# Optimization experiments

Hardware: AMD Instinct MI355X
Metric: run time of the kernel (lower is better)

## Reference

```python
import jax, jax.numpy as jnp
import numpy as np

NHEAD = 8; DM = 512; DFF = 2048; L = 4; S = 1024; NTOK = 51; MLP = 256; CLASSES = 7
GH = 3; GHID = 64; GCLS = 5; ALPHA = 0.2
HD = DM // NHEAD

_ADJ = np.array([[0,1,0,0,0],[1,1,1,1,0],[1,0,1,0,1],[1,0,0,1,1],[0,0,1,1,1]], dtype=np.int32)


def setup_inputs():
    key = jax.random.key(0)
    ks = jax.random.split(key, 24)
    r = lambda k, s, sc=0.05: jax.random.normal(k, s, jnp.float32) * sc
    return {
        'x': jax.random.normal(ks[0], (5, S, NTOK), jnp.float32),
        'adj': jnp.asarray(_ADJ),
        'W_enc': r(ks[1], (NTOK, DM)), 'b_enc': jnp.zeros((DM,), jnp.float32),
        'cls_tok': r(ks[2], (1, 1, DM)),
        'pos_emb': r(ks[3], (S + 1, DM)),
        'Wq': r(ks[4], (L, DM, DM)), 'bq': jnp.zeros((L, DM), jnp.float32),
        'Wk': r(ks[5], (L, DM, DM)), 'bk': jnp.zeros((L, DM), jnp.float32),
        'Wv': r(ks[6], (L, DM, DM)), 'bv': jnp.zeros((L, DM), jnp.float32),
        'Wo': r(ks[7], (L, DM, DM)), 'bo': jnp.zeros((L, DM), jnp.float32),
        'W1': r(ks[8], (L, DM, DFF)), 'b1': jnp.zeros((L, DFF), jnp.float32),
        'W2': r(ks[9], (L, DFF, DM)), 'b2': jnp.zeros((L, DM), jnp.float32),
        'g1': jnp.ones((L, DM), jnp.float32), 'be1': jnp.zeros((L, DM), jnp.float32),
        'g2': jnp.ones((L, DM), jnp.float32), 'be2': jnp.zeros((L, DM), jnp.float32),
        'Wd1': r(ks[10], (DM, MLP)), 'bd1': jnp.zeros((MLP,), jnp.float32),
        'Wd2': r(ks[11], (MLP, CLASSES)), 'bd2': jnp.zeros((CLASSES,), jnp.float32),
        'Wg': r(ks[12], (GH, 3, GHID), 0.3), 'ag': r(ks[13], (GH, 2 * GHID), 0.3),
        'Wgo': r(ks[14], (GH * GHID, GCLS), 0.3), 'ago': r(ks[15], (2 * GCLS,), 0.3),
    }


def _layernorm(x, g, b, eps=1e-5):
    m = x.mean(-1, keepdims=True)
    v = ((x - m) ** 2).mean(-1, keepdims=True)
    return (x - m) * jax.lax.rsqrt(v + eps) * g + b


def _gat_attn_layer(h_in, W, a, mask):
    # standard pyGAT GraphAttentionLayer: e_ij = LeakyReLU(a1.h_i + a2.h_j)
    F = W.shape[1]
    h = h_in @ W                                                    # [N, F]
    e = jax.nn.leaky_relu((h @ a[:F])[:, None] + (h @ a[F:])[None, :], ALPHA)
    att = jax.nn.softmax(jnp.where(mask, e, -9e15), axis=-1)        # adjacency-masked softmax
    return att @ h


def _gat(xg, mask, Wg, ag, Wgo, ago):
    # xg: [5 nodes, 3 feats]; GH attention heads concatenated, then output layer
    heads = jax.vmap(lambda W, a: jax.nn.elu(_gat_attn_layer(xg, W, a, mask)))(Wg, ag)  # [GH,5,GHID]
    hcat = jnp.transpose(heads, (1, 0, 2)).reshape(xg.shape[0], GH * GHID)
    out = jax.nn.elu(_gat_attn_layer(hcat, Wgo, ago, mask))         # [5, GCLS]
    return jax.nn.log_softmax(out, axis=1)


def _forward(x, adj, params):
    (W_enc, b_enc, cls_tok, pos_emb, Wq, bq, Wk, bk, Wv, bv, Wo, bo,
     W1, b1, W2, b2, g1, be1, g2, be2, Wd1, bd1, Wd2, bd2, Wg, ag, Wgo, ago) = params
    mask = adj > 0
    # --- batched GAT: the source loops over T timesteps x 5 feature groups; here fully vectorized ---
    # x[:, :, :15] : batch(=5 nodes) x T x 15 -> [T*5groups, 5 nodes, 3]
    xg = x[:, :, :15].reshape(5, S, 5, 3)
    xg = jnp.transpose(xg, (1, 2, 0, 3)).reshape(S * 5, 5, 3)
    gat_out = jax.vmap(lambda g: _gat(g, mask, Wg, ag, Wgo, ago))(xg)
    gat_out = gat_out.reshape(S, 5, 5, GCLS)                        # [T, group, node, class]
    # --- transformer branch (eval mode: dropout = identity) ---
    h = x @ W_enc + b_enc                                           # [5, S, DM]
    h = jnp.concatenate([jnp.broadcast_to(cls_tok, (5, 1, DM)), h], axis=1)
    h = h + pos_emb[None]
    for i in range(L):
        q = (h @ Wq[i] + bq[i]).reshape(5, S + 1, NHEAD, HD)
        k = (h @ Wk[i] + bk[i]).reshape(5, S + 1, NHEAD, HD)
        v = (h @ Wv[i] + bv[i]).reshape(5, S + 1, NHEAD, HD)
        sc = jnp.einsum('bthd,bshd->bhts', q, k) / jnp.sqrt(jnp.float32(HD))
        att = jax.nn.softmax(sc, axis=-1)
        o = jnp.einsum('bhts,bshd->bthd', att, v).reshape(5, S + 1, DM) @ Wo[i] + bo[i]
        h = _layernorm(h + o, g1[i], be1[i])
        f = jax.nn.relu(h @ W1[i] + b1[i]) @ W2[i] + b2[i]
        h = _layernorm(h + f, g2[i], be2[i])
    cls = h[:, 0, :]                                                # lambda: x[:, 0, :]
    out = (cls @ Wd1 + bd1) @ Wd2 + bd2                             # no activation between dense layers (as in source)
    return out, gat_out


def reference(x, adj, W_enc, b_enc, cls_tok, pos_emb, Wq, bq, Wk, bk, Wv, bv, Wo, bo, W1, b1, W2, b2, g1, be1, g2, be2, Wd1, bd1, Wd2, bd2, Wg, ag, Wgo, ago):
    params = (W_enc, b_enc, cls_tok, pos_emb, Wq, bq, Wk, bk, Wv, bv, Wo, bo,
              W1, b1, W2, b2, g1, be1, g2, be2, Wd1, bd1, Wd2, bd2, Wg, ag, Wgo, ago)
    return _forward(x, adj, params)
```

## Files before the change

kernel.cpp:

```cpp
#include <hip/hip_runtime.h>
#include <hip/hip_bf16.h>
#include <math.h>

#define NBATCH 5
#define SEQ    1024
#define T      1025
#define ROWS   (NBATCH * T)
#define MP     5248
#define DM     512
#define DFF    2048
#define NHEAD  8
#define HD     64
#define NTOK   51
#define MLPDIM 256
#define NCLS   7
#define GH     3
#define GHID   64
#define GCLS   5
#define NGRAPH (SEQ * 5)
#define QKVN   1536
#define TPAD   1152

typedef __attribute__((ext_vector_type(8))) short bf16x8;
typedef __attribute__((ext_vector_type(4))) float f32x4;

#define GM_AS(p)  ((const __attribute__((address_space(1))) void*)(p))
#define LDS_AS(p) ((__attribute__((address_space(3))) void*)(p))

__device__ __forceinline__ unsigned short f2bf(float f) {
    unsigned int u = __float_as_uint(f);
    unsigned int r = (u + 0x7FFFu + ((u >> 16) & 1u)) >> 16;
    return (unsigned short)r;
}
__device__ __forceinline__ float bf2f(unsigned short u) {
    return __uint_as_float((unsigned int)u << 16);
}

__global__ __launch_bounds__(256) void setup_kernel(
    const float* __restrict__ Wq, const float* __restrict__ Wk,
    const float* __restrict__ Wv, const float* __restrict__ Wo_,
    const float* __restrict__ W1, const float* __restrict__ W2,
    const float* __restrict__ bq, const float* __restrict__ bk,
    const float* __restrict__ bv,
    unsigned short* __restrict__ Wqkvt, unsigned short* __restrict__ Wot,
    unsigned short* __restrict__ W1t, unsigned short* __restrict__ W2t,
    float* __restrict__ bqkv)
{
    int id = blockIdx.x;
    if (id >= 12288) {
        int i = id - 12288;
        #pragma unroll
        for (int rep = 0; rep < 2; ++rep) {
            int t = threadIdx.x + rep * 256;
            bqkv[i * QKVN + t]        = bq[i * DM + t];
            bqkv[i * QKVN + 512 + t]  = bk[i * DM + t];
            bqkv[i * QKVN + 1024 + t] = bv[i * DM + t];
        }
        return;
    }
    const float* W; unsigned short* Wt; int K, N, z, bx, by; long dstride;
    if (id < 4096) {
        int g = id >> 10, lid = id & 1023;
        K = DM; N = DM;
        z = lid >> 8; int r2 = lid & 255; by = r2 >> 4; bx = r2 & 15;
        if (g < 3) { W = (g == 0) ? Wq : (g == 1) ? Wk : Wv;
                     Wt = Wqkvt + (size_t)g * DM * DM; dstride = (long)QKVN * DM; }
        else       { W = Wo_; Wt = Wot; dstride = (long)DM * DM; }
    } else if (id < 8192) {
        int lid = id - 4096;
        K = DM; N = DFF;
        z = lid >> 10; int r2 = lid & 1023; by = r2 >> 6; bx = r2 & 63;
        W = W1; Wt = W1t; dstride = (long)DM * DFF;
    } else {
        int lid = id - 8192;
        K = DFF; N = DM;
        z = lid >> 10; int r2 = lid & 1023; by = r2 >> 4; bx = r2 & 15;
        W = W2; Wt = W2t; dstride = (long)DFF * DM;
    }
    const float* Wm = W + (size_t)z * K * N;
    unsigned short* Wo2 = Wt + (size_t)z * dstride;
    __shared__ float tile[32][33];
    int bX = bx * 32, bY = by * 32;
    int tx = threadIdx.x & 31, ty = threadIdx.x >> 5;
    #pragma unroll
    for (int i = 0; i < 32; i += 8)
        tile[ty + i][tx] = Wm[(size_t)(bY + ty + i) * N + bX + tx];
    __syncthreads();
    #pragma unroll
    for (int i = 0; i < 32; i += 8)
        Wo2[(size_t)(bX + ty + i) * K + bY + tx] = f2bf(tile[tx][ty + i]);
}

__global__ __launch_bounds__(256) void gemm_mfma(
    const unsigned short* __restrict__ A, const unsigned short* __restrict__ Bt,
    const float* __restrict__ bias, float* __restrict__ Cf,
    unsigned short* __restrict__ Cb, int N, int K, int relu)
{
    __shared__ unsigned short As[128 * 64];
    __shared__ unsigned short Bs[128 * 64];
    int tid = threadIdx.x;
    int l = tid & 63, w = tid >> 6;
    int wr = w & 1, wc = w >> 1;
    int mlane = l & 15, quad = l >> 4;
    int m0 = blockIdx.y * 128, n0 = blockIdx.x * 128;

    f32x4 acc[4][4] = {};

    for (int k0 = 0; k0 < K; k0 += 64) {
        __syncthreads();
        #pragma unroll
        for (int it = 0; it < 4; ++it) {
            int c = tid + it * 256;
            int row = c >> 3, cc = c & 7;
            const unsigned short* ga = A  + (size_t)(m0 + row) * K + k0 + cc * 8;
            __builtin_amdgcn_global_load_lds(GM_AS(ga), LDS_AS(As + c * 8), 16, 0, 0);
            const unsigned short* gb = Bt + (size_t)(n0 + row) * K + k0 + cc * 8;
            __builtin_amdgcn_global_load_lds(GM_AS(gb), LDS_AS(Bs + c * 8), 16, 0, 0);
        }
        __syncthreads();
        #pragma unroll
        for (int half = 0; half < 2; ++half) {
            int ko = half * 32 + quad * 8;
            bf16x8 afrag[4], bfrag[4];
            #pragma unroll
            for (int mi = 0; mi < 4; ++mi)
                afrag[mi] = *(const bf16x8*)(As + (wr * 64 + mi * 16 + mlane) * 64 + ko);
            #pragma unroll
            for (int ni = 0; ni < 4; ++ni)
                bfrag[ni] = *(const bf16x8*)(Bs + (wc * 64 + ni * 16 + mlane) * 64 + ko);
            #pragma unroll
            for (int mi = 0; mi < 4; ++mi)
                #pragma unroll
                for (int ni = 0; ni < 4; ++ni)
                    acc[mi][ni] = __builtin_amdgcn_mfma_f32_16x16x32_bf16(
                        afrag[mi], bfrag[ni], acc[mi][ni], 0, 0, 0);
        }
    }

    #pragma unroll
    for (int mi = 0; mi < 4; ++mi) {
        #pragma unroll
        for (int r = 0; r < 4; ++r) {
            int gm = m0 + wr * 64 + mi * 16 + quad * 4 + r;
            size_t rowoff = (size_t)gm * N;
            #pragma unroll
            for (int ni = 0; ni < 4; ++ni) {
                int gn = n0 + wc * 64 + ni * 16 + mlane;
                float val = acc[mi][ni][r] + bias[gn];
                if (relu) val = fmaxf(val, 0.f);
                if (Cb) Cb[rowoff + gn] = f2bf(val);
                else    Cf[rowoff + gn] = val;
            }
        }
    }
}

__global__ __launch_bounds__(256) void gemm_mfma_sk(
    const unsigned short* __restrict__ A, const unsigned short* __restrict__ Bt,
    unsigned short* __restrict__ part, int N, int K)
{
    __shared__ unsigned short As[128 * 64];
    __shared__ unsigned short Bs[128 * 64];
    int tid = threadIdx.x;
    int l = tid & 63, w = tid >> 6;
    int wr = w & 1, wc = w >> 1;
    int mlane = l & 15, quad = l >> 4;
    int m0 = blockIdx.y * 128, n0 = blockIdx.x * 128;
    int kper = K / gridDim.z;
    int kbeg = blockIdx.z * kper;

    f32x4 acc[4][4] = {};

    for (int k0 = kbeg; k0 < kbeg + kper; k0 += 64) {
        __syncthreads();
        #pragma unroll
        for (int it = 0; it < 4; ++it) {
            int c = tid + it * 256;
            int row = c >> 3, cc = c & 7;
            const unsigned short* ga = A  + (size_t)(m0 + row) * K + k0 + cc * 8;
            __builtin_amdgcn_global_load_lds(GM_AS(ga), LDS_AS(As + c * 8), 16, 0, 0);
            const unsigned short* gb = Bt + (size_t)(n0 + row) * K + k0 + cc * 8;
            __builtin_amdgcn_global_load_lds(GM_AS(gb), LDS_AS(Bs + c * 8), 16, 0, 0);
        }
        __syncthreads();
        #pragma unroll
        for (int half = 0; half < 2; ++half) {
            int ko = half * 32 + quad * 8;
            bf16x8 afrag[4], bfrag[4];
            #pragma unroll
            for (int mi = 0; mi < 4; ++mi)
                afrag[mi] = *(const bf16x8*)(As + (wr * 64 + mi * 16 + mlane) * 64 + ko);
            #pragma unroll
            for (int ni = 0; ni < 4; ++ni)
                bfrag[ni] = *(const bf16x8*)(Bs + (wc * 64 + ni * 16 + mlane) * 64 + ko);
            #pragma unroll
            for (int mi = 0; mi < 4; ++mi)
                #pragma unroll
                for (int ni = 0; ni < 4; ++ni)
                    acc[mi][ni] = __builtin_amdgcn_mfma_f32_16x16x32_bf16(
                        afrag[mi], bfrag[ni], acc[mi][ni], 0, 0, 0);
        }
    }

    unsigned short* pz = part + (size_t)blockIdx.z * MP * N;
    #pragma unroll
    for (int mi = 0; mi < 4; ++mi) {
        #pragma unroll
        for (int r = 0; r < 4; ++r) {
            int gm = m0 + wr * 64 + mi * 16 + quad * 4 + r;
            size_t rowoff = (size_t)gm * N;
            #pragma unroll
            for (int ni = 0; ni < 4; ++ni) {
                int gn = n0 + wc * 64 + ni * 16 + mlane;
                pz[rowoff + gn] = f2bf(acc[mi][ni][r]);
            }
        }
    }
}

__global__ __launch_bounds__(256) void vtrans_kernel(
    const unsigned short* __restrict__ vb, unsigned short* __restrict__ vt, int qs)
{
    __shared__ unsigned short tile[64][72];
    int bh = blockIdx.y;
    int b = bh >> 3, h = bh & 7;
    int t0 = blockIdx.x * 64;
    int tid = threadIdx.x;
    #pragma unroll
    for (int it = 0; it < 2; ++it) {
        int c = tid + it * 256;
        int key = c >> 3, cc = c & 7;
        int gk = t0 + key; if (gk >= T) gk = T - 1;
        *(bf16x8*)(&tile[key][cc * 8]) =
            *(const bf16x8*)(vb + ((size_t)b * T + gk) * qs + h * HD + cc * 8);
    }
    __syncthreads();
    #pragma unroll
    for (int it = 0; it < 2; ++it) {
        int c = tid + it * 256;
        int d = c >> 3, cc = c & 7;
        unsigned short tmp[8];
        #pragma unroll
        for (int j = 0; j < 8; ++j) tmp[j] = tile[cc * 8 + j][d];
        *(bf16x8*)(vt + ((size_t)bh * 64 + d) * TPAD + t0 + cc * 8) = *(bf16x8*)tmp;
    }
}

#define AQT 64
#define NR 9
__global__ __launch_bounds__(256) void attn_mfma(
    const unsigned short* __restrict__ qb, const unsigned short* __restrict__ kb,
    const unsigned short* __restrict__ vt, unsigned short* __restrict__ ob,
    int qs)
{
    __shared__ unsigned short Ks[128 * 72];
    __shared__ unsigned short Vs[64 * 136];
    __shared__ unsigned short Ps[4][16 * 72];
    int bh = blockIdx.y;
    int b = bh >> 3, h = bh & 7;
    int t0 = blockIdx.x * AQT;
    int tid = threadIdx.x;
    int l = tid & 63, w = tid >> 6;
    int ml = l & 15, quad = l >> 4;
    size_t rowbase = (size_t)b * T;
    const unsigned short* vtb = vt + (size_t)bh * 64 * TPAD;

    int qrow = t0 + w * 16 + ml; if (qrow >= T) qrow = T - 1;
    const unsigned short* qp = qb + (rowbase + qrow) * qs + h * HD + quad * 8;
    bf16x8 qf0 = *(const bf16x8*)qp;
    bf16x8 qf1 = *(const bf16x8*)(qp + 32);

    int krow = tid >> 3, kcc = tid & 7;
    int vd   = tid >> 4, vck = tid & 15;

    f32x4 oacc[4] = {};
    float lrow[4] = {0.f, 0.f, 0.f, 0.f};

    bf16x8 kr[4], vr[4];
    #pragma unroll
    for (int i = 0; i < 4; ++i) {
        int gk = krow + i * 32; if (gk >= T) gk = T - 1;
        kr[i] = *(const bf16x8*)(kb + (rowbase + gk) * qs + h * HD + kcc * 8);
        vr[i] = *(const bf16x8*)(vtb + (size_t)(vd + i * 16) * TPAD + vck * 8);
    }

    for (int rnd = 0; rnd < NR; ++rnd) {
        int c0 = rnd * 128;
        __syncthreads();
        #pragma unroll
        for (int i = 0; i < 4; ++i) {
            *(bf16x8*)(Ks + (krow + i * 32) * 72 + kcc * 8) = kr[i];
            *(bf16x8*)(Vs + (vd + i * 16) * 136 + vck * 8) = vr[i];
        }
        __syncthreads();
        if (rnd + 1 < NR) {
            int n0k = c0 + 128;
            #pragma unroll
            for (int i = 0; i < 4; ++i) {
                int gk = n0k + krow + i * 32; if (gk >= T) gk = T - 1;
                kr[i] = *(const bf16x8*)(kb + (rowbase + gk) * qs + h * HD + kcc * 8);
                vr[i] = *(const bf16x8*)(vtb + (size_t)(vd + i * 16) * TPAD + n0k + vck * 8);
            }
        }

        #pragma unroll
        for (int p = 0; p < 2; ++p) {
            int kb0 = p * 64;
            f32x4 s[4] = {};
            #pragma unroll
            for (int ni = 0; ni < 4; ++ni) {
                const unsigned short* kfp = Ks + (kb0 + ni * 16 + ml) * 72 + quad * 8;
                bf16x8 kf0 = *(const bf16x8*)kfp;
                bf16x8 kf1 = *(const bf16x8*)(kfp + 32);
                s[ni] = __builtin_amdgcn_mfma_f32_16x16x32_bf16(qf0, kf0, s[ni], 0, 0, 0);
                s[ni] = __builtin_amdgcn_mfma_f32_16x16x32_bf16(qf1, kf1, s[ni], 0, 0, 0);
            }
            #pragma unroll
            for (int ni = 0; ni < 4; ++ni) {
                bool valid = (c0 + kb0 + ni * 16 + ml) < T;
                #pragma unroll
                for (int r = 0; r < 4; ++r) {
                    float pv = valid ? __expf(s[ni][r] * 0.125f) : 0.f;
                    s[ni][r] = pv;
                    lrow[r] += pv;
                }
            }
            unsigned short* pw = Ps[w];
            #pragma unroll
            for (int r = 0; r < 4; ++r)
                #pragma unroll
                for (int ni = 0; ni < 4; ++ni)
                    pw[(quad * 4 + r) * 72 + ((ni * 16 + ml) ^ (quad << 4))] = f2bf(s[ni][r]);
            int sw = ((ml >> 2) & 3) << 4;
            #pragma unroll
            for (int kc = 0; kc < 2; ++kc) {
                bf16x8 pf = *(const bf16x8*)(pw + ml * 72 + ((kc * 32 + quad * 8) ^ sw));
                #pragma unroll
                for (int ni = 0; ni < 4; ++ni) {
                    bf16x8 vf = *(const bf16x8*)(Vs + (ni * 16 + ml) * 136 + kb0 + kc * 32 + quad * 8);
                    oacc[ni] = __builtin_amdgcn_mfma_f32_16x16x32_bf16(pf, vf, oacc[ni], 0, 0, 0);
                }
            }
        }
    }

    #pragma unroll
    for (int r = 0; r < 4; ++r) {
        #pragma unroll
        for (int off = 1; off < 16; off <<= 1)
            lrow[r] += __shfl_xor(lrow[r], off);
    }
    #pragma unroll
    for (int r = 0; r < 4; ++r) {
        int grow = t0 + w * 16 + quad * 4 + r;
        if (grow >= T) continue;
        float inv = 1.f / lrow[r];
        unsigned short* op = ob + (rowbase + grow) * DM + h * HD;
        #pragma unroll
        for (int ni = 0; ni < 4; ++ni)
            op[ni * 16 + ml] = f2bf(oacc[ni][r] * inv);
    }
}

__global__ __launch_bounds__(256) void encoder_kernel(
    const float* __restrict__ x, const float* __restrict__ W_enc,
    const float* __restrict__ b_enc, const float* __restrict__ cls_tok,
    const float* __restrict__ pos_emb, float* __restrict__ h,
    unsigned short* __restrict__ hb)
{
    int row = blockIdx.x;
    int b = row / T, tt = row % T;
    int tid = threadIdx.x;
    float* hp = h + (size_t)row * DM;
    unsigned short* hbp = hb + (size_t)row * DM;
    if (tt == 0) {
        float a0 = cls_tok[tid]       + pos_emb[tid];
        float a1 = cls_tok[tid + 256] + pos_emb[tid + 256];
        hp[tid] = a0; hp[tid + 256] = a1;
        hbp[tid] = f2bf(a0); hbp[tid + 256] = f2bf(a1);
        return;
    }
    __shared__ float xs[NTOK];
    int s = tt - 1;
    if (tid < NTOK) xs[tid] = x[((size_t)b * SEQ + s) * NTOK + tid];
    __syncthreads();
    #pragma unroll
    for (int rep = 0; rep < 2; ++rep) {
        int d = tid + rep * 256;
        float acc = b_enc[d] + pos_emb[(size_t)tt * DM + d];
        for (int kx = 0; kx < NTOK; ++kx) acc += xs[kx] * W_enc[kx * DM + d];
        hp[d] = acc;
        hbp[d] = f2bf(acc);
    }
}

__global__ __launch_bounds__(256) void add_lnp_kernel(
    float* __restrict__ h, const unsigned short* __restrict__ part, int np,
    const float* __restrict__ bias, const float* __restrict__ g,
    const float* __restrict__ be, unsigned short* __restrict__ hb)
{
    int w = threadIdx.x >> 6, l = threadIdx.x & 63;
    int row = blockIdx.x * 4 + w;
    if (row >= ROWS) return;
    float* hp = h + (size_t)row * DM + l * 8;
    unsigned short* hbp = hb + (size_t)row * DM + l * 8;
    float4 a0 = *(const float4*)(hp);
    float4 a1 = *(const float4*)(hp + 4);
    float4 b0 = *(const float4*)(bias + l * 8);
    float4 b1 = *(const float4*)(bias + l * 8 + 4);
    float v[8] = {a0.x + b0.x, a0.y + b0.y, a0.z + b0.z, a0.w + b0.w,
                  a1.x + b1.x, a1.y + b1.y, a1.z + b1.z, a1.w + b1.w};
    for (int pp = 0; pp < np; ++pp) {
        const unsigned short* prp = part + ((size_t)pp * MP + row) * DM + l * 8;
        bf16x8 pv = *(const bf16x8*)prp;
        #pragma unroll
        for (int i = 0; i < 8; ++i) v[i] += bf2f((unsigned short)pv[i]);
    }
    float s = 0.f;
    #pragma unroll
    for (int i = 0; i < 8; ++i) s += v[i];
    #pragma unroll
    for (int off = 1; off < 64; off <<= 1) s += __shfl_xor(s, off);
    float mean = s * (1.f / DM);
    float sq = 0.f;
    #pragma unroll
    for (int i = 0; i < 8; ++i) { v[i] -= mean; sq += v[i] * v[i]; }
    #pragma unroll
    for (int off = 1; off < 64; off <<= 1) sq += __shfl_xor(sq, off);
    float inv = rsqrtf(sq * (1.f / DM) + 1e-5f);
    float4 g0 = *(const float4*)(g + l * 8);
    float4 g1 = *(const float4*)(g + l * 8 + 4);
    float4 e0 = *(const float4*)(be + l * 8);
    float4 e1 = *(const float4*)(be + l * 8 + 4);
    float o[8];
    o[0] = v[0]*inv*g0.x + e0.x; o[1] = v[1]*inv*g0.y + e0.y;
    o[2] = v[2]*inv*g0.z + e0.z; o[3] = v[3]*inv*g0.w + e0.w;
    o[4] = v[4]*inv*g1.x + e1.x; o[5] = v[5]*inv*g1.y + e1.y;
    o[6] = v[6]*inv*g1.z + e1.z; o[7] = v[7]*inv*g1.w + e1.w;
    *(float4*)(hp)     = make_float4(o[0], o[1], o[2], o[3]);
    *(float4*)(hp + 4) = make_float4(o[4], o[5], o[6], o[7]);
    ushort4 p0 = {f2bf(o[0]), f2bf(o[1]), f2bf(o[2]), f2bf(o[3])};
    ushort4 p1 = {f2bf(o[4]), f2bf(o[5]), f2bf(o[6]), f2bf(o[7])};
    *(ushort4*)(hbp)     = p0;
    *(ushort4*)(hbp + 4) = p1;
}

__global__ __launch_bounds__(256) void dec1_kernel(
    const float* __restrict__ h, const float* __restrict__ Wd1,
    float* __restrict__ part)
{
    int kc = blockIdx.x, b = blockIdx.y, tid = threadIdx.x;
    __shared__ float cs[64];
    const float* cls = h + (size_t)b * T * DM;
    if (tid < 64) cs[tid] = cls[kc * 64 + tid];
    __syncthreads();
    float acc = 0.f;
    #pragma unroll
    for (int kx = 0; kx < 64; ++kx)
        acc += cs[kx] * Wd1[(size_t)(kc * 64 + kx) * MLPDIM + tid];
    part[(size_t)(b * 8 + kc) * MLPDIM + tid] = acc;
}

__global__ __launch_bounds__(256) void dec2_kernel(
    const float* __restrict__ part, const float* __restrict__ bd1,
    const float* __restrict__ Wd2, const float* __restrict__ bd2,
    float* __restrict__ out)
{
    __shared__ float t1s[MLPDIM];
    int tid = threadIdx.x;
    for (int b = 0; b < NBATCH; ++b) {
        float acc = bd1[tid];
        #pragma unroll
        for (int kc = 0; kc < 8; ++kc)
            acc += part[(size_t)(b * 8 + kc) * MLPDIM + tid];
        t1s[tid] = acc;
        __syncthreads();
        if (tid < NCLS) {
            float a2 = bd2[tid];
            for (int kx = 0; kx < MLPDIM; ++kx) a2 += t1s[kx] * Wd2[kx * NCLS + tid];
            out[b * NCLS + tid] = a2;
        }
        __syncthreads();
    }
}

__global__ __launch_bounds__(64) void gat_kernel(
    const float* __restrict__ x, const int* __restrict__ adj,
    const float* __restrict__ Wg, const float* __restrict__ ag,
    const float* __restrict__ Wgo, const float* __restrict__ ago,
    float* __restrict__ out)
{
    int g = blockIdx.x;
    int s = g / 5, jj = g % 5;
    int tid = threadIdx.x;
    __shared__ float xs[5][3];
    __shared__ int adjs[25];
    __shared__ float hb[GH][5][GHID + 1];
    __shared__ float o1[GH][5][GHID + 1];
    __shared__ float srcb[GH][5], dstb[GH][5];
    __shared__ float attb[GH][5][5];
    __shared__ float h2[5][5], src2[5], dst2[5], att2[5][5], o2[5][5];

    if (tid < 15) { int n = tid / 3, c = tid % 3;
        xs[n][c] = x[(size_t)n * SEQ * NTOK + (size_t)s * NTOK + jj * 3 + c]; }
    if (tid < 25) adjs[tid] = adj[tid];
    __syncthreads();

    #pragma unroll
    for (int hh = 0; hh < GH; ++hh)
        #pragma unroll
        for (int n = 0; n < 5; ++n)
            hb[hh][n][tid] = xs[n][0] * Wg[hh * 192 + tid]
                           + xs[n][1] * Wg[hh * 192 + 64 + tid]
                           + xs[n][2] * Wg[hh * 192 + 128 + tid];
    __syncthreads();

    if (tid < 15) { int hh = tid / 5, n = tid % 5; float a = 0.f;
        for (int f = 0; f < GHID; ++f) a += hb[hh][n][f] * ag[hh * 128 + f];
        srcb[hh][n] = a;
    } else if (tid >= 32 && tid < 47) { int t2 = tid - 32; int hh = t2 / 5, n = t2 % 5; float a = 0.f;
        for (int f = 0; f < GHID; ++f) a += hb[hh][n][f] * ag[hh * 128 + 64 + f];
        dstb[hh][n] = a;
    }
    __syncthreads();

    if (tid < 15) { int hh = tid / 5, i = tid % 5;
        float e[5]; float mx = -1e30f;
        #pragma unroll
        for (int j2 = 0; j2 < 5; ++j2) {
            float ev = srcb[hh][i] + dstb[hh][j2];
            ev = ev > 0.f ? ev : 0.2f * ev;
            e[j2] = ev;
            if (adjs[i * 5 + j2] && ev > mx) mx = ev;
        }
        float sum = 0.f;
        #pragma unroll
        for (int j2 = 0; j2 < 5; ++j2) {
            float p = adjs[i * 5 + j2] ? expf(e[j2] - mx) : 0.f;
            e[j2] = p; sum += p;
        }
        float inv = 1.f / sum;
        #pragma unroll
        for (int j2 = 0; j2 < 5; ++j2) attb[hh][i][j2] = e[j2] * inv;
    }
    __syncthreads();

    #pragma unroll
    for (int hh = 0; hh < GH; ++hh)
        #pragma unroll
        for (int n = 0; n < 5; ++n) {
            float a = 0.f;
            #pragma unroll
            for (int j2 = 0; j2 < 5; ++j2) a += attb[hh][n][j2] * hb[hh][j2][tid];
            o1[hh][n][tid] = a > 0.f ? a : expm1f(a);
        }
    __syncthreads();

    if (tid < 25) { int n = tid / 5, m = tid % 5; float a = 0.f;
        for (int hh = 0; hh < GH; ++hh)
            for (int f = 0; f < GHID; ++f)
                a += o1[hh][n][f] * Wgo[(hh * GHID + f) * GCLS + m];
        h2[n][m] = a;
    }
    __syncthreads();

    if (tid < 5) { float a = 0.f;
        for (int m = 0; m < GCLS; ++m) a += h2[tid][m] * ago[m];
        src2[tid] = a;
    } else if (tid >= 8 && tid < 13) { int n = tid - 8; float a = 0.f;
        for (int m = 0; m < GCLS; ++m) a += h2[n][m] * ago[GCLS + m];
        dst2[n] = a;
    }
    __syncthreads();

    if (tid < 5) { int i = tid;
        float e[5]; float mx = -1e30f;
        #pragma unroll
        for (int j2 = 0; j2 < 5; ++j2) {
            float ev = src2[i] + dst2[j2];
            ev = ev > 0.f ? ev : 0.2f * ev;
            e[j2] = ev;
            if (adjs[i * 5 + j2] && ev > mx) mx = ev;
        }
        float sum = 0.f;
        #pragma unroll
        for (int j2 = 0; j2 < 5; ++j2) {
            float p = adjs[i * 5 + j2] ? expf(e[j2] - mx) : 0.f;
            e[j2] = p; sum += p;
        }
        float inv = 1.f / sum;
        #pragma unroll
        for (int j2 = 0; j2 < 5; ++j2) att2[i][j2] = e[j2] * inv;
    }
    __syncthreads();

    if (tid < 25) { int n = tid / 5, m = tid % 5; float a = 0.f;
        #pragma unroll
        for (int j2 = 0; j2 < 5; ++j2) a += att2[n][j2] * h2[j2][m];
        o2[n][m] = a > 0.f ? a : expm1f(a);
    }
    __syncthreads();

    if (tid < 5) { int n = tid;
        float mx = o2[n][0];
        #pragma unroll
        for (int m = 1; m < GCLS; ++m) mx = fmaxf(mx, o2[n][m]);
        float sum = 0.f;
        #pragma unroll
        for (int m = 0; m < GCLS; ++m) sum += expf(o2[n][m] - mx);
        float ls = logf(sum);
        #pragma unroll
        for (int m = 0; m < GCLS; ++m)
            out[(size_t)g * 25 + n * 5 + m] = o2[n][m] - mx - ls;
    }
}

extern "C" void kernel_launch(void* const* d_in, const int* in_sizes, int n_in,
                              void* d_out, int out_size, void* d_ws, size_t ws_size,
                              hipStream_t stream)
{
    const float* x       = (const float*)d_in[0];
    const int*   adj     = (const int*)  d_in[1];
    const float* W_enc   = (const float*)d_in[2];
    const float* b_enc   = (const float*)d_in[3];
    const float* cls_tok = (const float*)d_in[4];
    const float* pos_emb = (const float*)d_in[5];
    const float* Wq = (const float*)d_in[6];
    const float* bq = (const float*)d_in[7];
    const float* Wk = (const float*)d_in[8];
    const float* bk = (const float*)d_in[9];
    const float* Wv = (const float*)d_in[10];
    const float* bv = (const float*)d_in[11];
    const float* Wo = (const float*)d_in[12];
    const float* bo = (const float*)d_in[13];
    const float* W1 = (const float*)d_in[14];
    const float* b1 = (const float*)d_in[15];
    const float* W2 = (const float*)d_in[16];
    const float* b2 = (const float*)d_in[17];
    const float* g1 = (const float*)d_in[18];
    const float* be1= (const float*)d_in[19];
    const float* g2 = (const float*)d_in[20];
    const float* be2= (const float*)d_in[21];
    const float* Wd1= (const float*)d_in[22];
    const float* bd1= (const float*)d_in[23];
    const float* Wd2= (const float*)d_in[24];
    const float* bd2= (const float*)d_in[25];
    const float* Wg = (const float*)d_in[26];
    const float* ag = (const float*)d_in[27];
    const float* Wgo= (const float*)d_in[28];
    const float* ago= (const float*)d_in[29];
    float* out = (float*)d_out;

    float* ws = (float*)d_ws;
    float* h = ws;
    unsigned short* hb   = (unsigned short*)(h + (size_t)MP * DM);
    unsigned short* qkvb = hb + (size_t)MP * DM;
    unsigned short* ob   = qkvb + (size_t)MP * QKVN;
    unsigned short* f1b  = qkvb;
    unsigned short* Wqkvt= ob + (size_t)MP * DM;
    unsigned short* Wot  = Wqkvt + (size_t)4 * QKVN * DM;
    unsigned short* W1t  = Wot + (size_t)4 * DM * DM;
    unsigned short* W2t  = W1t + (size_t)4 * DM * DFF;
    float* bqkv = (float*)(W2t + (size_t)4 * DFF * DM);
    float* dpart = bqkv + 4 * QKVN;
    unsigned short* vt = (unsigned short*)(dpart + NBATCH * 8 * MLPDIM);
    unsigned short* parts = vt + (size_t)40 * 64 * TPAD;

    setup_kernel<<<12292, 256, 0, stream>>>(Wq, Wk, Wv, Wo, W1, W2, bq, bk, bv,
                                            Wqkvt, Wot, W1t, W2t, bqkv);

    gat_kernel<<<NGRAPH, 64, 0, stream>>>(x, adj, Wg, ag, Wgo, ago, out + NBATCH * NCLS);
    encoder_kernel<<<ROWS, 256, 0, stream>>>(x, W_enc, b_enc, cls_tok, pos_emb, h, hb);

    dim3 gqkv (QKVN / 128, MP / 128);
    dim3 g2048(DFF / 128, MP / 128);
    dim3 gWo  (DM / 128, MP / 128, 2);
    dim3 gW2  (DM / 128, MP / 128, 4);
    dim3 gAttn(17, NBATCH * NHEAD);
    dim3 gVt  (TPAD / 64, NBATCH * NHEAD);
    int gLN = (ROWS + 3) / 4;

    for (int i = 0; i < 4; ++i) {
        gemm_mfma<<<gqkv, 256, 0, stream>>>(hb, Wqkvt + (size_t)i*QKVN*DM, bqkv + i*QKVN, nullptr, qkvb, QKVN, DM, 0);
        vtrans_kernel<<<gVt, 256, 0, stream>>>(qkvb + 1024, vt, QKVN);
        attn_mfma<<<gAttn, 256, 0, stream>>>(qkvb, qkvb + 512, vt, ob, QKVN);
        gemm_mfma_sk<<<gWo, 256, 0, stream>>>(ob, Wot + (size_t)i*DM*DM, parts, DM, DM);
        add_lnp_kernel<<<gLN, 256, 0, stream>>>(h, parts, 2, bo + i*DM, g1 + i*DM, be1 + i*DM, hb);
        gemm_mfma<<<g2048, 256, 0, stream>>>(hb,  W1t + (size_t)i*DM*DFF, b1 + i*DFF, nullptr, f1b, DFF, DM, 1);
        gemm_mfma_sk<<<gW2, 256, 0, stream>>>(f1b, W2t + (size_t)i*DM*DFF, parts, DM, DFF);
        add_lnp_kernel<<<gLN, 256, 0, stream>>>(h, parts, 4, b2 + i*DM, g2 + i*DM, be2 + i*DM, hb);
    }

    dec1_kernel<<<dim3(8, NBATCH), 256, 0, stream>>>(h, Wd1, dpart);
    dec2_kernel<<<1, 256, 0, stream>>>(dpart, bd1, Wd2, bd2, out);
}
```

Baseline: 801.3 us.

## Fuse V transpose into QKV GEMM, peel tail key, batch encoder rows, merge decoder

```diff
diff --git a/kernel.cpp b/kernel.cpp
--- a/kernel.cpp
+++ b/kernel.cpp
@@ -94,7 +94,8 @@
 __global__ __launch_bounds__(256) void gemm_mfma(
     const unsigned short* __restrict__ A, const unsigned short* __restrict__ Bt,
     const float* __restrict__ bias, float* __restrict__ Cf,
-    unsigned short* __restrict__ Cb, int N, int K, int relu)
+    unsigned short* __restrict__ Cb, unsigned short* __restrict__ Vt,
+    int N, int K, int relu)
 {
     __shared__ unsigned short As[128 * 64];
     __shared__ unsigned short Bs[128 * 64];
@@ -148,8 +149,14 @@
                 int gn = n0 + wc * 64 + ni * 16 + mlane;
                 float val = acc[mi][ni][r] + bias[gn];
                 if (relu) val = fmaxf(val, 0.f);
-                if (Cb) Cb[rowoff + gn] = f2bf(val);
-                else    Cf[rowoff + gn] = val;
+                if (Vt && gn >= 1024) {
+                    int bb = gm / T;
+                    if (bb < NBATCH) {
+                        int tt = gm - bb * T;
+                        Vt[((size_t)(bb * 512 + (gn - 1024))) * TPAD + tt] = f2bf(val);
+                    }
+                } else if (Cb) Cb[rowoff + gn] = f2bf(val);
+                else           Cf[rowoff + gn] = val;
             }
         }
     }
@@ -218,36 +225,8 @@
     }
 }
 
-__global__ __launch_bounds__(256) void vtrans_kernel(
-    const unsigned short* __restrict__ vb, unsigned short* __restrict__ vt, int qs)
-{
-    __shared__ unsigned short tile[64][72];
-    int bh = blockIdx.y;
-    int b = bh >> 3, h = bh & 7;
-    int t0 = blockIdx.x * 64;
-    int tid = threadIdx.x;
-    #pragma unroll
-    for (int it = 0; it < 2; ++it) {
-        int c = tid + it * 256;
-        int key = c >> 3, cc = c & 7;
-        int gk = t0 + key; if (gk >= T) gk = T - 1;
-        *(bf16x8*)(&tile[key][cc * 8]) =
-            *(const bf16x8*)(vb + ((size_t)b * T + gk) * qs + h * HD + cc * 8);
-    }
-    __syncthreads();
-    #pragma unroll
-    for (int it = 0; it < 2; ++it) {
-        int c = tid + it * 256;
-        int d = c >> 3, cc = c & 7;
-        unsigned short tmp[8];
-        #pragma unroll
-        for (int j = 0; j < 8; ++j) tmp[j] = tile[cc * 8 + j][d];
-        *(bf16x8*)(vt + ((size_t)bh * 64 + d) * TPAD + t0 + cc * 8) = *(bf16x8*)tmp;
-    }
-}
-
 #define AQT 64
-#define NR 9
+#define NR 8
 __global__ __launch_bounds__(256) void attn_mfma(
     const unsigned short* __restrict__ qb, const unsigned short* __restrict__ kb,
     const unsigned short* __restrict__ vt, unsigned short* __restrict__ ob,
@@ -256,9 +235,11 @@
     __shared__ unsigned short Ks[128 * 72];
     __shared__ unsigned short Vs[64 * 136];
     __shared__ unsigned short Ps[4][16 * 72];
-    int bh = blockIdx.y;
+    int flat = blockIdx.y * 17 + blockIdx.x;
+    int wi = flat >> 3;
+    int bh = (flat & 7) + ((wi / 17) << 3);
+    int t0 = (wi % 17) * AQT;
     int b = bh >> 3, h = bh & 7;
-    int t0 = blockIdx.x * AQT;
     int tid = threadIdx.x;
     int l = tid & 63, w = tid >> 6;
     int ml = l & 15, quad = l >> 4;
@@ -279,13 +260,12 @@
     bf16x8 kr[4], vr[4];
     #pragma unroll
     for (int i = 0; i < 4; ++i) {
-        int gk = krow + i * 32; if (gk >= T) gk = T - 1;
+        int gk = krow + i * 32;
         kr[i] = *(const bf16x8*)(kb + (rowbase + gk) * qs + h * HD + kcc * 8);
         vr[i] = *(const bf16x8*)(vtb + (size_t)(vd + i * 16) * TPAD + vck * 8);
     }
 
     for (int rnd = 0; rnd < NR; ++rnd) {
-        int c0 = rnd * 128;
         __syncthreads();
         #pragma unroll
         for (int i = 0; i < 4; ++i) {
@@ -294,10 +274,10 @@
         }
         __syncthreads();
         if (rnd + 1 < NR) {
-            int n0k = c0 + 128;
+            int n0k = (rnd + 1) * 128;
             #pragma unroll
             for (int i = 0; i < 4; ++i) {
-                int gk = n0k + krow + i * 32; if (gk >= T) gk = T - 1;
+                int gk = n0k + krow + i * 32;
                 kr[i] = *(const bf16x8*)(kb + (rowbase + gk) * qs + h * HD + kcc * 8);
                 vr[i] = *(const bf16x8*)(vtb + (size_t)(vd + i * 16) * TPAD + n0k + vck * 8);
             }
@@ -317,10 +297,9 @@
             }
             #pragma unroll
             for (int ni = 0; ni < 4; ++ni) {
-                bool valid = (c0 + kb0 + ni * 16 + ml) < T;
                 #pragma unroll
                 for (int r = 0; r < 4; ++r) {
-                    float pv = valid ? __expf(s[ni][r] * 0.125f) : 0.f;
+                    float pv = __expf(s[ni][r] * 0.125f);
                     s[ni][r] = pv;
                     lrow[r] += pv;
                 }
@@ -350,6 +329,34 @@
         for (int off = 1; off < 16; off <<= 1)
             lrow[r] += __shfl_xor(lrow[r], off);
     }
+
+    {
+        const unsigned short* kp = kb + (rowbase + SEQ) * qs + h * HD + quad * 8;
+        bf16x8 kf0 = *(const bf16x8*)kp;
+        bf16x8 kf1 = *(const bf16x8*)(kp + 32);
+        float dot = 0.f;
+        #pragma unroll
+        for (int j = 0; j < 8; ++j) {
+            dot += bf2f((unsigned short)qf0[j]) * bf2f((unsigned short)kf0[j]);
+            dot += bf2f((unsigned short)qf1[j]) * bf2f((unsigned short)kf1[j]);
+        }
+        dot += __shfl_xor(dot, 16);
+        dot += __shfl_xor(dot, 32);
+        float pe = __expf(dot * 0.125f);
+        float vv[4];
+        #pragma unroll
+        for (int ni = 0; ni < 4; ++ni)
+            vv[ni] = bf2f(vtb[(size_t)(ni * 16 + ml) * TPAD + SEQ]);
+        #pragma unroll
+        for (int r = 0; r < 4; ++r) {
+            float pr = __shfl(pe, quad * 4 + r);
+            lrow[r] += pr;
+            #pragma unroll
+            for (int ni = 0; ni < 4; ++ni)
+                oacc[ni][r] += pr * vv[ni];
+        }
+    }
+
     #pragma unroll
     for (int r = 0; r < 4; ++r) {
         int grow = t0 + w * 16 + quad * 4 + r;
@@ -362,35 +369,54 @@
     }
 }
 
+#define ENC_RPB 8
 __global__ __launch_bounds__(256) void encoder_kernel(
     const float* __restrict__ x, const float* __restrict__ W_enc,
     const float* __restrict__ b_enc, const float* __restrict__ cls_tok,
     const float* __restrict__ pos_emb, float* __restrict__ h,
     unsigned short* __restrict__ hb)
 {
-    int row = blockIdx.x;
-    int b = row / T, tt = row % T;
+    int r0 = blockIdx.x * ENC_RPB;
     int tid = threadIdx.x;
-    float* hp = h + (size_t)row * DM;
-    unsigned short* hbp = hb + (size_t)row * DM;
-    if (tt == 0) {
-        float a0 = cls_tok[tid]       + pos_emb[tid];
-        float a1 = cls_tok[tid + 256] + pos_emb[tid + 256];
-        hp[tid] = a0; hp[tid + 256] = a1;
-        hbp[tid] = f2bf(a0); hbp[tid + 256] = f2bf(a1);
-        return;
-    }
-    __shared__ float xs[NTOK];
-    int s = tt - 1;
-    if (tid < NTOK) xs[tid] = x[((size_t)b * SEQ + s) * NTOK + tid];
+    __shared__ float xs[ENC_RPB][NTOK + 1];
+    for (int i = tid; i < ENC_RPB * NTOK; i += 256) {
+        int rr = i / NTOK, c = i % NTOK;
+        int row = r0 + rr;
+        float v = 0.f;
+        if (row < ROWS) {
+            int b = row / T, tt = row % T;
+            if (tt > 0)
+                v = x[((size_t)b * SEQ + (tt - 1)) * NTOK + c];
+        }
+        xs[rr][c] = v;
+    }
     __syncthreads();
     #pragma unroll
     for (int rep = 0; rep < 2; ++rep) {
         int d = tid + rep * 256;
-        float acc = b_enc[d] + pos_emb[(size_t)tt * DM + d];
-        for (int kx = 0; kx < NTOK; ++kx) acc += xs[kx] * W_enc[kx * DM + d];
-        hp[d] = acc;
-        hbp[d] = f2bf(acc);
+        float acc[ENC_RPB];
+        #pragma unroll
+        for (int rr = 0; rr < ENC_RPB; ++rr) acc[rr] = 0.f;
+        for (int kx = 0; kx < NTOK; ++kx) {
+            float wv = W_enc[kx * DM + d];
+            #pragma unroll
+            for (int rr = 0; rr < ENC_RPB; ++rr)
+                acc[rr] += xs[rr][kx] * wv;
+        }
+        float be = b_enc[d];
+        float ct = cls_tok[d];
+        #pragma unroll
+        for (int rr = 0; rr < ENC_RPB; ++rr) {
+            int row = r0 + rr;
+            if (row < ROWS) {
+                int b = row / T, tt = row % T;
+                float res;
+                if (tt == 0) res = ct + pos_emb[d];
+                else         res = acc[rr] + be + pos_emb[(size_t)tt * DM + d];
+                h[(size_t)row * DM + d]  = res;
+                hb[(size_t)row * DM + d] = f2bf(res);
+            }
+        }
     }
 }
 
@@ -445,42 +471,28 @@
     *(ushort4*)(hbp + 4) = p1;
 }
 
-__global__ __launch_bounds__(256) void dec1_kernel(
+__global__ __launch_bounds__(256) void dec_kernel(
     const float* __restrict__ h, const float* __restrict__ Wd1,
-    float* __restrict__ part)
-{
-    int kc = blockIdx.x, b = blockIdx.y, tid = threadIdx.x;
-    __shared__ float cs[64];
+    const float* __restrict__ bd1, const float* __restrict__ Wd2,
+    const float* __restrict__ bd2, float* __restrict__ out)
+{
+    int b = blockIdx.x;
+    int tid = threadIdx.x;
+    __shared__ float cs[DM];
+    __shared__ float t1s[MLPDIM];
     const float* cls = h + (size_t)b * T * DM;
-    if (tid < 64) cs[tid] = cls[kc * 64 + tid];
-    __syncthreads();
-    float acc = 0.f;
-    #pragma unroll
-    for (int kx = 0; kx < 64; ++kx)
-        acc += cs[kx] * Wd1[(size_t)(kc * 64 + kx) * MLPDIM + tid];
-    part[(size_t)(b * 8 + kc) * MLPDIM + tid] = acc;
-}
-
-__global__ __launch_bounds__(256) void dec2_kernel(
-    const float* __restrict__ part, const float* __restrict__ bd1,
-    const float* __restrict__ Wd2, const float* __restrict__ bd2,
-    float* __restrict__ out)
-{
-    __shared__ float t1s[MLPDIM];
-    int tid = threadIdx.x;
-    for (int b = 0; b < NBATCH; ++b) {
-        float acc = bd1[tid];
-        #pragma unroll
-        for (int kc = 0; kc < 8; ++kc)
-            acc += part[(size_t)(b * 8 + kc) * MLPDIM + tid];
-        t1s[tid] = acc;
-        __syncthreads();
-        if (tid < NCLS) {
-            float a2 = bd2[tid];
-            for (int kx = 0; kx < MLPDIM; ++kx) a2 += t1s[kx] * Wd2[kx * NCLS + tid];
-            out[b * NCLS + tid] = a2;
-        }
-        __syncthreads();
+    cs[tid]       = cls[tid];
+    cs[tid + 256] = cls[tid + 256];
+    __syncthreads();
+    float acc = bd1[tid];
+    for (int kx = 0; kx < DM; ++kx)
+        acc += cs[kx] * Wd1[(size_t)kx * MLPDIM + tid];
+    t1s[tid] = acc;
+    __syncthreads();
+    if (tid < NCLS) {
+        float a2 = bd2[tid];
+        for (int kx = 0; kx < MLPDIM; ++kx) a2 += t1s[kx] * Wd2[kx * NCLS + tid];
+        out[b * NCLS + tid] = a2;
     }
 }
 
@@ -670,27 +682,25 @@
                                             Wqkvt, Wot, W1t, W2t, bqkv);
 
     gat_kernel<<<NGRAPH, 64, 0, stream>>>(x, adj, Wg, ag, Wgo, ago, out + NBATCH * NCLS);
-    encoder_kernel<<<ROWS, 256, 0, stream>>>(x, W_enc, b_enc, cls_tok, pos_emb, h, hb);
+    encoder_kernel<<<(ROWS + ENC_RPB - 1) / ENC_RPB, 256, 0, stream>>>(
+        x, W_enc, b_enc, cls_tok, pos_emb, h, hb);
 
     dim3 gqkv (QKVN / 128, MP / 128);
     dim3 g2048(DFF / 128, MP / 128);
     dim3 gWo  (DM / 128, MP / 128, 2);
     dim3 gW2  (DM / 128, MP / 128, 4);
     dim3 gAttn(17, NBATCH * NHEAD);
-    dim3 gVt  (TPAD / 64, NBATCH * NHEAD);
     int gLN = (ROWS + 3) / 4;
 
     for (int i = 0; i < 4; ++i) {
-        gemm_mfma<<<gqkv, 256, 0, stream>>>(hb, Wqkvt + (size_t)i*QKVN*DM, bqkv + i*QKVN, nullptr, qkvb, QKVN, DM, 0);
-        vtrans_kernel<<<gVt, 256, 0, stream>>>(qkvb + 1024, vt, QKVN);
+        gemm_mfma<<<gqkv, 256, 0, stream>>>(hb, Wqkvt + (size_t)i*QKVN*DM, bqkv + i*QKVN, nullptr, qkvb, vt, QKVN, DM, 0);
         attn_mfma<<<gAttn, 256, 0, stream>>>(qkvb, qkvb + 512, vt, ob, QKVN);
         gemm_mfma_sk<<<gWo, 256, 0, stream>>>(ob, Wot + (size_t)i*DM*DM, parts, DM, DM);
         add_lnp_kernel<<<gLN, 256, 0, stream>>>(h, parts, 2, bo + i*DM, g1 + i*DM, be1 + i*DM, hb);
-        gemm_mfma<<<g2048, 256, 0, stream>>>(hb,  W1t + (size_t)i*DM*DFF, b1 + i*DFF, nullptr, f1b, DFF, DM, 1);
+        gemm_mfma<<<g2048, 256, 0, stream>>>(hb,  W1t + (size_t)i*DM*DFF, b1 + i*DFF, nullptr, f1b, nullptr, DFF, DM, 1);
         gemm_mfma_sk<<<gW2, 256, 0, stream>>>(f1b, W2t + (size_t)i*DM*DFF, parts, DM, DFF);
         add_lnp_kernel<<<gLN, 256, 0, stream>>>(h, parts, 4, b2 + i*DM, g2 + i*DM, be2 + i*DM, hb);
     }
 
-    dec1_kernel<<<dim3(8, NBATCH), 256, 0, stream>>>(h, Wd1, dpart);
-    dec2_kernel<<<1, 256, 0, stream>>>(dpart, bd1, Wd2, bd2, out);
-}
+    dec_kernel<<<NBATCH, 256, 0, stream>>>(h, Wd1, bd1, Wd2, bd2, out);
+}
```

Result: no change. 817.0 us (+2.0%).
